# Optimization experiments

Measured on AMD Instinct MI355X. Metric: run time of the kernel, lower is better.

## Reference

```python
import jax, jax.numpy as jnp
import numpy as np

N = 1_000_000
E = 32_000_000

def setup_inputs() -> dict:
    key = jax.random.key(0)
    k = jax.random.split(key, 7)
    x = jax.random.normal(k[0], (N, 1), dtype=jnp.float32)
    edge_index = jax.random.randint(k[1], (2, E), 0, N, dtype=jnp.int64)
    # lin1: 1 -> 4
    W1 = jax.random.normal(k[2], (4, 1), dtype=jnp.float32) * 0.5
    b1 = jax.random.normal(k[3], (4,), dtype=jnp.float32) * 0.1
    # lin2: 4 -> 1
    W2 = jax.random.normal(k[4], (1, 4), dtype=jnp.float32) * 0.5
    b2 = jax.random.normal(k[5], (1,), dtype=jnp.float32) * 0.1
    # SAGEConv lin_l: 1 -> 1, no bias, no root weight
    Wsage = jax.random.normal(k[6], (1, 1), dtype=jnp.float32) * 0.5
    return {"x": x, "edge_index": edge_index, "W1": W1, "b1": b1,
            "W2": W2, "b2": b2, "Wsage": Wsage}

def reference(x, edge_index, W1, b1, W2, b2, Wsage):
    # tiny MLP: 1 -> 4 -> 1
    h = jax.nn.relu(x @ W1.T + b1)          # [N,4]
    h = h @ W2.T + b2                        # [N,1]
    # SAGEConv mean aggregation: edges flow src -> dst
    src, dst = edge_index[0], edge_index[1]
    n = x.shape[0]
    agg = jax.ops.segment_sum(h[src], dst, num_segments=n)          # [N,1]
    cnt = jax.ops.segment_sum(jnp.ones((src.shape[0], 1), h.dtype), dst,
                              num_segments=n)                        # [N,1]
    mean = agg / jnp.maximum(cnt, 1.0)       # isolated nodes -> 0 (PyG behavior)
    return mean @ Wsage.T                    # lin_l, no root weight, no bias
```

## Files before the change

kernel.cpp:

```cpp
#include <hip/hip_runtime.h>
#include <hip/hip_fp16.h>


#define NBINS    256
#define BSHIFT   12
#define DMASK    4095
#define NBLK     512
#define STHREADS 512
#define EPT      16
#define TILE     (STHREADS * EPT)
#define PACK_SCALE 1048576.0

__global__ void detect_dtype_kernel(const int* __restrict__ ei, int* __restrict__ flag) {
    if (threadIdx.x == 0 && blockIdx.x == 0) {
        int is64 = 1;
        for (int i = 1; i < 256; i += 2) {
            if (ei[i] != 0) { is64 = 0; break; }
        }
        *flag = is64;
    }
}

__global__ void node_kernel(const float* __restrict__ x,
                            const float* __restrict__ W1,
                            const float* __restrict__ b1,
                            const float* __restrict__ W2,
                            const float* __restrict__ b2,
                            unsigned short* __restrict__ h2f16,
                            int n) {
    int i = blockIdx.x * blockDim.x + threadIdx.x;
    if (i >= n) return;
    float xi = x[i];
    float acc = b2[0];
#pragma unroll
    for (int j = 0; j < 4; ++j) {
        float t = fmaxf(W1[j] * xi + b1[j], 0.0f);
        acc += W2[j] * t;
    }
    h2f16[i] = __half_as_ushort(__float2half(acc));
}

__global__ void __launch_bounds__(STHREADS)
scatter_tile_kernel(const int* __restrict__ ei,
                    const unsigned short* __restrict__ h2f16,
                    unsigned int* __restrict__ entries,
                    int* __restrict__ index,
                    const int* __restrict__ flag,
                    long long E, long long chunk, int tpb, int ntiles) {
    __shared__ unsigned int ents[TILE];
    __shared__ int hist[NBINS];
    __shared__ int scanbuf[NBINS];
    __shared__ int toff[NBINS];

    const int t = threadIdx.x;
    long long start = (long long)blockIdx.x * chunk;
    long long end   = start + chunk; if (end > E) end = E;
    const int is64 = *flag;
    const long long* e64 = (const long long*)ei;

    int ti = 0;
    for (long long tbase = start; tbase < end; tbase += TILE, ++ti) {
        for (int i = t; i < NBINS; i += STHREADS) hist[i] = 0;
        __syncthreads();

        int sk[EPT], dk[EPT];
        if (is64) {
#pragma unroll
            for (int k = 0; k < EPT; ++k) {
                long long e = tbase + (long long)k * STHREADS + t;
                if (e < end) {
                    sk[k] = (int)__builtin_nontemporal_load(&e64[e]);
                    dk[k] = (int)__builtin_nontemporal_load(&e64[E + e]);
                } else { sk[k] = 0; dk[k] = -1; }
            }
        } else {
#pragma unroll
            for (int k = 0; k < EPT; ++k) {
                long long e = tbase + (long long)k * STHREADS + t;
                if (e < end) {
                    sk[k] = __builtin_nontemporal_load(&ei[e]);
                    dk[k] = __builtin_nontemporal_load(&ei[E + e]);
                } else { sk[k] = 0; dk[k] = -1; }
            }
        }

        unsigned int hv[EPT];
#pragma unroll
        for (int k = 0; k < EPT; ++k) hv[k] = (unsigned int)h2f16[sk[k]];

        int rk[EPT];
#pragma unroll
        for (int k = 0; k < EPT; ++k)
            if (dk[k] >= 0) rk[k] = atomicAdd(&hist[dk[k] >> BSHIFT], 1);
        __syncthreads();

        if (t < NBINS) scanbuf[t] = hist[t];
        __syncthreads();
        for (int off = 1; off < NBINS; off <<= 1) {
            int v = 0;
            if (t < NBINS && t >= off) v = scanbuf[t - off];
            __syncthreads();
            if (t < NBINS) scanbuf[t] += v;
            __syncthreads();
        }
        if (t < NBINS) toff[t] = scanbuf[t] - hist[t];
        __syncthreads();

#pragma unroll
        for (int k = 0; k < EPT; ++k) {
            if (dk[k] >= 0) {
                int slot = toff[dk[k] >> BSHIFT] + rk[k];
                ents[slot] = ((unsigned int)(dk[k] & DMASK) << 16) | hv[k];
            }
        }
        __syncthreads();

        const int tilecount = scanbuf[NBINS - 1];
        const int g = blockIdx.x * tpb + ti;
        unsigned int* gout = entries + (long long)g * TILE;
        for (int j = t; j < tilecount; j += STHREADS)
            __builtin_nontemporal_store(ents[j], &gout[j]);
        if (t < NBINS)
            __builtin_nontemporal_store(toff[t], &index[(long long)t * ntiles + g]);
        else if (t == NBINS)
            __builtin_nontemporal_store(tilecount, &index[(long long)NBINS * ntiles + g]);
        __syncthreads();
    }
}

__global__ void __launch_bounds__(1024, 8)
aggregate_kernel(const unsigned int* __restrict__ entries,
                 const int* __restrict__ index,
                 double* __restrict__ partial,
                 int ntiles) {
    __shared__ double acc[4096];
    const int b   = blockIdx.x >> 1;
    const int sub = blockIdx.x & 1;
    const int t   = threadIdx.x;
    for (int i = t; i < 4096; i += blockDim.x) acc[i] = 0.0;
    __syncthreads();

    const int half_t = ntiles >> 1;
    const int gbase  = sub * half_t;
    const int wave = t >> 6;
    const int lane = t & 63;
    const int half = lane >> 5;
    const int hl   = lane & 31;
    const int* __restrict__ rowS = index + (long long)b * ntiles;
    const int* __restrict__ rowE = index + (long long)(b + 1) * ntiles;

    for (int g = gbase + wave * 2 + half; g < gbase + half_t; g += 32) {
        int s = rowS[g];
        int e = rowE[g];
        const unsigned int* run = entries + (long long)g * TILE;
        for (int i = s + hl; i < e; i += 32) {
            unsigned int ent = __builtin_nontemporal_load(&run[i]);
            int dlow = (int)(ent >> 16);
            float v  = __half2float(__ushort_as_half((unsigned short)(ent & 0xFFFFu)));
            atomicAdd(&acc[dlow], (double)v + PACK_SCALE);
        }
    }
    __syncthreads();

    double* p = partial + (long long)blockIdx.x * 4096;
    for (int i = t; i < 4096; i += blockDim.x)
        __builtin_nontemporal_store(acc[i], &p[i]);
}

__global__ void finalize_kernel(const double* __restrict__ partial,
                                const float* __restrict__ Wsage,
                                float* __restrict__ out,
                                int n) {
    int i = blockIdx.x * blockDim.x + threadIdx.x;
    if (i >= n) return;
    int b    = i >> BSHIFT;
    int dlow = i & DMASK;
    double v = partial[(long long)(b * 2) * 4096 + dlow]
             + partial[(long long)(b * 2 + 1) * 4096 + dlow];
    double cnt = nearbyint(v * (1.0 / PACK_SCALE));
    double agg = v - cnt * PACK_SCALE;
    out[i] = (float)(agg / fmax(cnt, 1.0)) * Wsage[0];
}


__global__ void node_f32_kernel(const float* __restrict__ x,
                                const float* __restrict__ W1,
                                const float* __restrict__ b1,
                                const float* __restrict__ W2,
                                const float* __restrict__ b2,
                                float* __restrict__ h2,
                                int n) {
    int i = blockIdx.x * blockDim.x + threadIdx.x;
    if (i >= n) return;
    float xi = x[i];
    float acc = b2[0];
#pragma unroll
    for (int j = 0; j < 4; ++j) {
        float t = fmaxf(W1[j] * xi + b1[j], 0.0f);
        acc += W2[j] * t;
    }
    h2[i] = acc;
}

__global__ void zero_packed_kernel(double* __restrict__ packed, int n) {
    int i = blockIdx.x * blockDim.x + threadIdx.x;
    if (i < n) packed[i] = 0.0;
}

__global__ void edge_atomic_kernel(const int* __restrict__ ei,
                                   const float* __restrict__ h2,
                                   double* __restrict__ packed,
                                   const int* __restrict__ flag,
                                   long long E) {
    long long i      = (long long)blockIdx.x * blockDim.x + threadIdx.x;
    long long stride = (long long)gridDim.x * blockDim.x;
    const int is64 = *flag;
    if (is64) {
        const long long* e64 = (const long long*)ei;
        for (long long e = i; e < E; e += stride) {
            int s = (int)e64[e];
            int d = (int)e64[E + e];
            atomicAdd(&packed[d], (double)h2[s] + PACK_SCALE);
        }
    } else {
        for (long long e = i; e < E; e += stride) {
            int s = ei[e];
            int d = ei[E + e];
            atomicAdd(&packed[d], (double)h2[s] + PACK_SCALE);
        }
    }
}

__global__ void out_packed_kernel(const double* __restrict__ packed,
                                  const float* __restrict__ Wsage,
                                  float* __restrict__ out,
                                  int n) {
    int i = blockIdx.x * blockDim.x + threadIdx.x;
    if (i >= n) return;
    double v   = packed[i];
    double cnt = nearbyint(v * (1.0 / PACK_SCALE));
    double agg = v - cnt * PACK_SCALE;
    out[i] = (float)(agg / fmax(cnt, 1.0)) * Wsage[0];
}

extern "C" void kernel_launch(void* const* d_in, const int* in_sizes, int n_in,
                              void* d_out, int out_size, void* d_ws, size_t ws_size,
                              hipStream_t stream) {
    const float* x     = (const float*)d_in[0];
    const int*   ei    = (const int*)d_in[1];
    const float* W1    = (const float*)d_in[2];
    const float* b1    = (const float*)d_in[3];
    const float* W2    = (const float*)d_in[4];
    const float* b2    = (const float*)d_in[5];
    const float* Wsage = (const float*)d_in[6];

    const int       n = in_sizes[0];
    const long long E = (long long)in_sizes[1] / 2;

    const long long chunk  = (E + NBLK - 1) / NBLK;
    const int       tpb    = (int)((chunk + TILE - 1) / TILE);
    const int       ntiles = NBLK * tpb;

    const size_t entries_b = (size_t)ntiles * TILE * 4;
    const size_t index_b   = (size_t)(NBINS + 1) * ntiles * 4;
    const size_t partial_b = (size_t)2 * NBINS * 4096 * 8;
    const size_t h2_b      = (size_t)n * 2;
    const size_t need      = entries_b + index_b + partial_b + h2_b + 64;

    if (ws_size >= need) {
        unsigned int*   entries = (unsigned int*)d_ws;
        int*            index   = (int*)((char*)d_ws + entries_b);
        double*         partial = (double*)((char*)d_ws + entries_b + index_b);
        unsigned short* h2f16   = (unsigned short*)((char*)d_ws + entries_b + index_b + partial_b);
        int*            flag    = (int*)((char*)d_ws + entries_b + index_b + partial_b + h2_b);

        detect_dtype_kernel<<<1, 64, 0, stream>>>(ei, flag);
        {
            int threads = 256;
            int blocks  = (n + threads - 1) / threads;
            node_kernel<<<blocks, threads, 0, stream>>>(x, W1, b1, W2, b2, h2f16, n);
        }
        scatter_tile_kernel<<<NBLK, STHREADS, 0, stream>>>(ei, h2f16, entries, index,
                                                           flag, E, chunk, tpb, ntiles);
        aggregate_kernel<<<NBINS * 2, 1024, 0, stream>>>(entries, index, partial, ntiles);
        {
            int threads = 256;
            int blocks  = (n + threads - 1) / threads;
            finalize_kernel<<<blocks, threads, 0, stream>>>(partial, Wsage,
                                                            (float*)d_out, n);
        }
    } else {
        double* packed = (double*)d_ws;
        float*  h2     = (float*)d_out;
        int*    flag   = (int*)(packed + n);

        detect_dtype_kernel<<<1, 64, 0, stream>>>(ei, flag);
        {
            int threads = 256;
            int blocks  = (n + threads - 1) / threads;
            node_f32_kernel<<<blocks, threads, 0, stream>>>(x, W1, b1, W2, b2, h2, n);
            zero_packed_kernel<<<blocks, threads, 0, stream>>>(packed, n);
        }
        edge_atomic_kernel<<<4096, 256, 0, stream>>>(ei, h2, packed, flag, E);
        {
            int threads = 256;
            int blocks  = (n + threads - 1) / threads;
            out_packed_kernel<<<blocks, threads, 0, stream>>>(packed, Wsage,
                                                              (float*)d_out, n);
        }
    }
}
```

Measured before the change: 314.4 us.

## Replace block-wide scan with single-wavefront shuffle scan and double scatter blocks

The 256-bin exclusive scan in the scatter kernel used a Hillis-Steele loop with many block-wide barriers. It now runs in one 64-lane wavefront: each lane sums four bins and the lanes scan with __shfl_up, so only one barrier is needed. The scatter grid size NBLK is also doubled to 1024 blocks, giving more parallelism with fewer tiles per block, at the cost of more partially filled tiles and a larger index array.

```diff
diff --git a/kernel.cpp b/kernel.cpp
--- a/kernel.cpp
+++ b/kernel.cpp
@@ -5,7 +5,7 @@
 #define NBINS    256
 #define BSHIFT   12
 #define DMASK    4095
-#define NBLK     512
+#define NBLK     1024
 #define STHREADS 512
 #define EPT      16
 #define TILE     (STHREADS * EPT)
@@ -49,8 +49,8 @@
                     long long E, long long chunk, int tpb, int ntiles) {
     __shared__ unsigned int ents[TILE];
     __shared__ int hist[NBINS];
-    __shared__ int scanbuf[NBINS];
     __shared__ int toff[NBINS];
+    __shared__ int s_total;
 
     const int t = threadIdx.x;
     long long start = (long long)blockIdx.x * chunk;
@@ -94,16 +94,24 @@
             if (dk[k] >= 0) rk[k] = atomicAdd(&hist[dk[k] >> BSHIFT], 1);
         __syncthreads();
 
-        if (t < NBINS) scanbuf[t] = hist[t];
-        __syncthreads();
-        for (int off = 1; off < NBINS; off <<= 1) {
-            int v = 0;
-            if (t < NBINS && t >= off) v = scanbuf[t - off];
-            __syncthreads();
-            if (t < NBINS) scanbuf[t] += v;
-            __syncthreads();
-        }
-        if (t < NBINS) toff[t] = scanbuf[t] - hist[t];
+        if (t < 64) {
+            const int base = t * 4;
+            int a0 = hist[base], a1 = hist[base + 1],
+                a2 = hist[base + 2], a3 = hist[base + 3];
+            int s  = a0 + a1 + a2 + a3;
+            int sc = s;
+#pragma unroll
+            for (int off = 1; off < 64; off <<= 1) {
+                int up = __shfl_up(sc, off, 64);
+                if (t >= off) sc += up;
+            }
+            int excl = sc - s;
+            toff[base]     = excl;
+            toff[base + 1] = excl + a0;
+            toff[base + 2] = excl + a0 + a1;
+            toff[base + 3] = excl + a0 + a1 + a2;
+            if (t == 63) s_total = sc;
+        }
         __syncthreads();
 
 #pragma unroll
@@ -115,7 +123,7 @@
         }
         __syncthreads();
 
-        const int tilecount = scanbuf[NBINS - 1];
+        const int tilecount = s_total;
         const int g = blockIdx.x * tpb + ti;
         unsigned int* gout = entries + (long long)g * TILE;
         for (int j = t; j < tilecount; j += STHREADS)
```

New measurement: 310.8 us. About the same (-1.2%).
